# Kernel tuning notes

Hardware: AMD Instinct MI355X
Metric: run time of the kernel (lower is better)

Reference implementation:

```python
import jax, jax.numpy as jnp
import numpy as np

B, T, H, V, ADIM, AMAX = 16, 1024, 512, 32000, 512, 10


def setup_inputs() -> dict:
    key = jax.random.key(0)
    ks = jax.random.split(key, 24)
    def n(k, shape, s=0.05):
        return jax.random.normal(k, shape, jnp.float32) * s
    return {
        "instruction": jax.random.randint(ks[0], (B, T), 0, V, dtype=jnp.int32),
        "emb": n(ks[1], (V, H)),
        "wih_f": n(ks[2], (4 * H, H)), "whh_f": n(ks[3], (4 * H, H)),
        "bih_f": n(ks[4], (4 * H,)), "bhh_f": n(ks[5], (4 * H,)),
        "wih_b": n(ks[6], (4 * H, H)), "whh_b": n(ks[7], (4 * H, H)),
        "bih_b": n(ks[8], (4 * H,)), "bhh_b": n(ks[9], (4 * H,)),
        "wg": n(ks[10], (2 * H, 2 * H)), "bg": n(ks[11], (2 * H,)),
        "ws1": n(ks[12], (H, 2 * H)), "bs1": n(ks[13], (H,)),
        "ws2": n(ks[14], (1, H)), "bs2": n(ks[15], (1,)),
        "wd1": n(ks[16], (H, 2 * H)), "bd1": n(ks[17], (H,)),
        "wd2": n(ks[18], (ADIM, H)), "bd2": n(ks[19], (ADIM,)),
        "max_actions": AMAX,
    }


def _lstm(x, wih, whh, bias):
    # x: [B, T, H] -> outputs [B, T, H]; PyTorch gate order i, f, g, o
    h0 = jnp.zeros((x.shape[0], whh.shape[1]), x.dtype)
    def step(carry, xt):
        h, c = carry
        g = xt @ wih.T + h @ whh.T + bias
        i, f, gg, o = jnp.split(g, 4, axis=-1)
        c = jax.nn.sigmoid(f) * c + jax.nn.sigmoid(i) * jnp.tanh(gg)
        h = jax.nn.sigmoid(o) * jnp.tanh(c)
        return (h, c), h
    _, hs = jax.lax.scan(step, (h0, h0), jnp.swapaxes(x, 0, 1))
    return jnp.swapaxes(hs, 0, 1)


def reference(instruction, emb, wih_f, whh_f, bih_f, bhh_f, wih_b, whh_b, bih_b, bhh_b,
              wg, bg, ws1, bs1, ws2, bs2, wd1, bd1, wd2, bd2, max_actions):
    x = emb[instruction]                                   # [B, T, H]
    fwd = _lstm(x, wih_f, whh_f, bih_f + bhh_f)            # [B, T, H]
    bwd = _lstm(x[:, ::-1], wih_b, whh_b, bih_b + bhh_b)[:, ::-1]
    enc = jnp.concatenate([fwd, bwd], axis=-1)             # [B, T, 2H]
    # sequence_lengths=None: h_n[0]=fwd last step, h_n[1]=bwd at t=0
    pooled = jnp.concatenate([fwd[:, -1], bwd[:, 0]], axis=-1)
    gctx = pooled @ wg.T + bg                               # [B, 2H]
    sh = jax.nn.relu(enc @ ws1.T + bs1)
    seg_probs = jax.nn.sigmoid((sh @ ws2.T + bs2)[..., 0])  # [B, T]
    mask = seg_probs > 0.5
    count = mask.sum(axis=-1)
    # first max_actions True positions per row (stable sort keeps time order)
    order = jnp.argsort(jnp.logical_not(mask), axis=1, stable=True)[:, :max_actions]
    gathered = jnp.take_along_axis(enc, order[..., None], axis=1)  # [B, A, 2H]
    slots = jnp.arange(max_actions)
    valid = slots[None, :] < jnp.minimum(count, max_actions)[:, None]
    empty = ((count == 0)[:, None]) & (slots[None, :] == 0)  # fallback: decode global ctx
    dec_in = jnp.where(valid[..., None], gathered, 0.0)
    dec_in = jnp.where(empty[..., None], gctx[:, None, :], dec_in)
    dh = jax.nn.relu(dec_in @ wd1.T + bd1)
    actions = (dh @ wd2.T + bd2) * (valid | empty)[..., None].astype(dec_in.dtype)
    return actions, seg_probs
```

## Files before the change

### kernel.cpp

```cpp
#include <hip/hip_runtime.h>
#include <math.h>

#define T   1024
#define NB  16
#define HD  512

#define OFF_BAR  0
#define OFF_HH   256
#define OFF_SH   (OFF_HH + 16777216)
#define OFF_SEGP (OFF_SH + 8388608)
#define OFF_GCTX (OFF_SEGP + 16384)
#define OFF_SEL  (OFF_GCTX + 16384)

typedef unsigned long long u64;

__device__ __forceinline__ float sigmoidf_(float x){ return 1.0f/(1.0f + __expf(-x)); }
__device__ __forceinline__ float tanhf_(float x){ return 1.0f - 2.0f/(1.0f + __expf(2.0f*x)); }

__global__ __launch_bounds__(512, 1)
void lstm_kernel(const int* __restrict__ instr, const float* __restrict__ emb,
                 const float* __restrict__ wih_f, const float* __restrict__ whh_f,
                 const float* __restrict__ bih_f, const float* __restrict__ bhh_f,
                 const float* __restrict__ wih_b, const float* __restrict__ whh_b,
                 const float* __restrict__ bih_b, const float* __restrict__ bhh_b,
                 float* __restrict__ ws)
{
    float* h_hist = ws + OFF_HH;
    int* flags = (int*)ws;

    const int wg    = blockIdx.x;
    const int dir   = wg & 1;
    const int slice = wg >> 1;
    const int U     = slice * 4;

    int* barf = flags + dir*128;

    const float* wih = dir ? wih_b : wih_f;
    const float* whh = dir ? whh_b : whh_f;
    const float* bih = dir ? bih_b : bih_f;
    const float* bhh = dir ? bhh_b : bhh_f;

    const int tid  = threadIdx.x;
    const int wid  = tid >> 6;
    const int lane = tid & 63;
    const int bg   = wid >> 1;
    const int rg   = wid & 1;

    float wi[64], wh[64];
#pragma unroll
    for (int ri = 0; ri < 8; ++ri){
        int rgl = rg*8 + ri;
        int gate = rgl >> 2, unit = rgl & 3;
        size_t row = (size_t)(gate*HD + U + unit) * HD + lane*8;
        float4 a0 = *(const float4*)(wih + row);
        float4 a1 = *(const float4*)(wih + row + 4);
        float4 b0 = *(const float4*)(whh + row);
        float4 b1 = *(const float4*)(whh + row + 4);
        wi[ri*8+0]=a0.x; wi[ri*8+1]=a0.y; wi[ri*8+2]=a0.z; wi[ri*8+3]=a0.w;
        wi[ri*8+4]=a1.x; wi[ri*8+5]=a1.y; wi[ri*8+6]=a1.z; wi[ri*8+7]=a1.w;
        wh[ri*8+0]=b0.x; wh[ri*8+1]=b0.y; wh[ri*8+2]=b0.z; wh[ri*8+3]=b0.w;
        wh[ri*8+4]=b1.x; wh[ri*8+5]=b1.y; wh[ri*8+6]=b1.z; wh[ri*8+7]=b1.w;
    }

    float bI, bF, bG, bO, cst = 0.0f;
    {
        int u = tid & 3;
        bI = bih[0*HD + U + u] + bhh[0*HD + U + u];
        bF = bih[1*HD + U + u] + bhh[1*HD + U + u];
        bG = bih[2*HD + U + u] + bhh[2*HD + U + u];
        bO = bih[3*HD + U + u] + bhh[3*HD + U + u];
    }

    __shared__ float gbuf[256];

    const int jown = ((lane&1)<<4)|((lane&2)<<2)|(lane&4)|((lane&8)>>2)|((lane&16)>>4);
    const int own_bi  = jown >> 3;
    const int own_rgl = rg*8 + (jown & 7);
    const int gslot   = (own_rgl >> 2)*64 + (bg*4 + own_bi)*4 + (own_rgl & 3);

    for (int s = 0; s < T; ++s){
        const int tp = dir ? (T-1-s) : s;

        float a[32];
#pragma unroll
        for (int j = 0; j < 32; ++j) a[j] = 0.0f;

#pragma unroll
        for (int bi = 0; bi < 4; ++bi){
            int b = bg*4 + bi;
            int idx = instr[b*T + tp];
            const float* px = emb + (size_t)idx*HD + lane*8;
            float4 x0 = *(const float4*)px;
            float4 x1 = *(const float4*)(px + 4);
            float xs[8] = {x0.x,x0.y,x0.z,x0.w,x1.x,x1.y,x1.z,x1.w};
#pragma unroll
            for (int kk = 0; kk < 8; ++kk){
                float xv = xs[kk];
#pragma unroll
                for (int ri = 0; ri < 8; ++ri)
                    a[bi*8+ri] = fmaf(xv, wi[ri*8+kk], a[bi*8+ri]);
            }
        }

        if (s > 0){
            if (wid == 0){
                for (;;){
                    int v0 = __hip_atomic_load((int*)(barf + lane),      __ATOMIC_RELAXED, __HIP_MEMORY_SCOPE_AGENT);
                    int v1 = __hip_atomic_load((int*)(barf + 64 + lane), __ATOMIC_RELAXED, __HIP_MEMORY_SCOPE_AGENT);
                    if (__all((v0 >= s) && (v1 >= s))) break;
                    __builtin_amdgcn_s_sleep(1);
                }
            }
            __syncthreads();

            const int tprev = dir ? (T - s) : (s - 1);
            const float* hbase = h_hist + (size_t)(dir*T + tprev)*NB*HD;
#pragma unroll
            for (int bi = 0; bi < 4; ++bi){
                int b = bg*4 + bi;
                const float* ph = hbase + (size_t)b*HD + lane*8;
                float4 h0 = *(const float4*)ph;
                float4 h1 = *(const float4*)(ph + 4);
                float hs[8] = {h0.x,h0.y,h0.z,h0.w,h1.x,h1.y,h1.z,h1.w};
#pragma unroll
                for (int kk = 0; kk < 8; ++kk){
                    float hv = hs[kk];
#pragma unroll
                    for (int ri = 0; ri < 8; ++ri)
                        a[bi*8+ri] = fmaf(hv, wh[ri*8+kk], a[bi*8+ri]);
                }
            }
        }

#pragma unroll
        for (int m = 0; m < 5; ++m){
            const int half = 16 >> m;
            const bool up = (lane >> m) & 1;
#pragma unroll
            for (int j = 0; j < 16; ++j){
                if (j < half){
                    float lo = a[j], hi = a[j+half];
                    float rlo = __shfl_xor(lo, 1<<m, 64);
                    float rhi = __shfl_xor(hi, 1<<m, 64);
                    a[j] = up ? (hi + rhi) : (lo + rlo);
                }
            }
        }
        a[0] += __shfl_xor(a[0], 32, 64);

        if ((lane & 32) == 0) gbuf[gslot] = a[0];
        __syncthreads();

        if (tid < 64){
            float iv = sigmoidf_(gbuf[      tid] + bI);
            float fv = sigmoidf_(gbuf[ 64 + tid] + bF);
            float gv = tanhf_  (gbuf[128 + tid] + bG);
            float ov = sigmoidf_(gbuf[192 + tid] + bO);
            cst = fv*cst + iv*gv;
            float hv = ov * tanhf_(cst);
            int b = tid >> 2, u = tid & 3;
            __hip_atomic_store(&h_hist[((size_t)(dir*T + tp)*NB + b)*HD + U + u], hv,
                               __ATOMIC_RELAXED, __HIP_MEMORY_SCOPE_AGENT);
        }
        asm volatile("s_waitcnt vmcnt(0)" ::: "memory");
        __builtin_amdgcn_sched_barrier(0);
        if (tid == 0)
            __hip_atomic_store(barf + slice, s + 1, __ATOMIC_RELAXED, __HIP_MEMORY_SCOPE_AGENT);
    }
}

__global__ __launch_bounds__(256, 2)
void seg_gemm(const float* __restrict__ ws_, const float* __restrict__ ws1,
              const float* __restrict__ bs1)
{
    const float* h_hist = ws_ + OFF_HH;
    float* SH = (float*)(ws_ + OFF_SH);
    __shared__ float As[64][17];
    __shared__ float Bs[64][17];
    const int m0 = blockIdx.x * 64;
    const int n0 = blockIdx.y * 64;
    const int tid = threadIdx.x;
    const int r  = tid >> 2;
    const int kq = (tid & 3) * 4;
    const int ty = tid >> 4, tx = tid & 15;
    const int bI = m0 >> 10;
    const int t0 = m0 & 1023;

    float acc[4][4];
#pragma unroll
    for (int i=0;i<4;i++)
#pragma unroll
        for (int j=0;j<4;j++) acc[i][j]=0.0f;

    for (int kb = 0; kb < 1024; kb += 16){
        int kk = kb + kq;
        const float* ap = (kk < 512)
            ? h_hist + ((size_t)(t0 + r)*NB + bI)*HD + kk
            : h_hist + ((size_t)(T + t0 + r)*NB + bI)*HD + (kk - 512);
        float4 av = *(const float4*)ap;
        As[r][kq+0]=av.x; As[r][kq+1]=av.y; As[r][kq+2]=av.z; As[r][kq+3]=av.w;
        float4 bv = *(const float4*)(ws1 + (size_t)(n0 + r)*1024 + kk);
        Bs[r][kq+0]=bv.x; Bs[r][kq+1]=bv.y; Bs[r][kq+2]=bv.z; Bs[r][kq+3]=bv.w;
        __syncthreads();
#pragma unroll
        for (int k2 = 0; k2 < 16; ++k2){
            float av_[4], bv_[4];
#pragma unroll
            for (int i=0;i<4;i++) av_[i] = As[ty*4+i][k2];
#pragma unroll
            for (int j=0;j<4;j++) bv_[j] = Bs[tx*4+j][k2];
#pragma unroll
            for (int i=0;i<4;i++)
#pragma unroll
                for (int j=0;j<4;j++) acc[i][j] = fmaf(av_[i], bv_[j], acc[i][j]);
        }
        __syncthreads();
    }
#pragma unroll
    for (int i=0;i<4;i++){
        int m = m0 + ty*4 + i;
#pragma unroll
        for (int j=0;j<4;j++){
            int n = n0 + tx*4 + j;
            SH[(size_t)m*512 + n] = fmaxf(acc[i][j] + bs1[n], 0.0f);
        }
    }
}

__global__ void seg_score(const float* __restrict__ ws_, const float* __restrict__ ws2,
                          const float* __restrict__ bs2, float* __restrict__ dout)
{
    const float* SH = ws_ + OFF_SH;
    float* segp = (float*)(ws_ + OFF_SEGP);
    int row  = blockIdx.x*4 + (threadIdx.x >> 6);
    int lane = threadIdx.x & 63;
    const float* p = SH + (size_t)row*512 + lane*8;
    const float* q = ws2 + lane*8;
    float4 a0=*(const float4*)p, a1=*(const float4*)(p+4);
    float4 b0=*(const float4*)q, b1=*(const float4*)(q+4);
    float ssum = a0.x*b0.x + a0.y*b0.y + a0.z*b0.z + a0.w*b0.w
               + a1.x*b1.x + a1.y*b1.y + a1.z*b1.z + a1.w*b1.w;
#pragma unroll
    for (int m=1;m<64;m<<=1) ssum += __shfl_xor(ssum, m, 64);
    if (lane == 0){
        float z = ssum + bs2[0];
        float pr = 1.0f/(1.0f + __expf(-z));
        segp[row] = pr;
        dout[81920 + row] = pr;
    }
}

__global__ void select_gctx(float* __restrict__ ws_, const float* __restrict__ wgm,
                            const float* __restrict__ bgv)
{
    const float* h_hist = ws_ + OFF_HH;
    const float* segp   = ws_ + OFF_SEGP;
    float* gctx = ws_ + OFF_GCTX;
    int* sel = (int*)(ws_ + OFF_SEL);
    int b = blockIdx.x, tid = threadIdx.x;
    __shared__ unsigned char flag[1024];
    __shared__ float pool[1024];
    for (int j = tid; j < 1024; j += 256){
        flag[j] = segp[b*1024 + j] > 0.5f ? 1 : 0;
        pool[j] = (j < 512) ? h_hist[((size_t)1023*NB + b)*HD + j]
                            : h_hist[((size_t)T*NB + b)*HD + (j - 512)];
    }
    __syncthreads();
    if (tid == 0){
        int c = 0;
        int tmp[10];
        for (int j = 0; j < 10; ++j) tmp[j] = 0;
        for (int t = 0; t < 1024; ++t){
            if (flag[t]){ if (c < 10) tmp[c] = t; c++; }
        }
        for (int j = 0; j < 10; ++j) sel[b*12 + j] = tmp[j];
        sel[b*12 + 10] = c;
        sel[b*12 + 11] = 0;
    }
    __syncthreads();
    for (int n = tid; n < 1024; n += 256){
        float acc = bgv[n];
        const float* wr = wgm + (size_t)n*1024;
        for (int k = 0; k < 1024; k += 4){
            acc += wr[k]*pool[k] + wr[k+1]*pool[k+1] + wr[k+2]*pool[k+2] + wr[k+3]*pool[k+3];
        }
        gctx[b*1024 + n] = acc;
    }
}

__global__ void decode(const float* __restrict__ ws_, const float* __restrict__ wd1,
                       const float* __restrict__ bd1, const float* __restrict__ wd2,
                       const float* __restrict__ bd2, float* __restrict__ dout)
{
    const float* h_hist = ws_ + OFF_HH;
    const float* gctx   = ws_ + OFF_GCTX;
    const int* sel = (const int*)(ws_ + OFF_SEL);
    int blk = blockIdx.x;
    int b = blk / 10, slot = blk % 10;
    int tid = threadIdx.x;
    int count = sel[b*12 + 10];
    int nval = count < 10 ? count : 10;
    bool empty = (count == 0);
    float* outp = dout + (size_t)(b*10 + slot)*512;
    if (slot >= nval && !(empty && slot == 0)){
        for (int n = tid; n < 512; n += 256) outp[n] = 0.0f;
        return;
    }
    __shared__ float row[1024];
    __shared__ float dh[512];
    if (empty){
        for (int j = tid; j < 1024; j += 256) row[j] = gctx[b*1024 + j];
    } else {
        int t = sel[b*12 + slot];
        for (int j = tid; j < 1024; j += 256)
            row[j] = (j < 512) ? h_hist[((size_t)t*NB + b)*HD + j]
                               : h_hist[((size_t)(T + t)*NB + b)*HD + (j-512)];
    }
    __syncthreads();
    for (int d = tid; d < 512; d += 256){
        float acc = bd1[d];
        const float* wr = wd1 + (size_t)d*1024;
        for (int k = 0; k < 1024; ++k) acc += wr[k]*row[k];
        dh[d] = fmaxf(acc, 0.0f);
    }
    __syncthreads();
    for (int n = tid; n < 512; n += 256){
        float acc = bd2[n];
        const float* wr = wd2 + (size_t)n*512;
        for (int k = 0; k < 512; ++k) acc += wr[k]*dh[k];
        outp[n] = acc;
    }
}

extern "C" void kernel_launch(void* const* d_in, const int* in_sizes, int n_in,
                              void* d_out, int out_size, void* d_ws, size_t ws_size,
                              hipStream_t stream)
{
    const int*   instr = (const int*)d_in[0];
    const float* emb   = (const float*)d_in[1];
    const float* wih_f = (const float*)d_in[2];
    const float* whh_f = (const float*)d_in[3];
    const float* bih_f = (const float*)d_in[4];
    const float* bhh_f = (const float*)d_in[5];
    const float* wih_b = (const float*)d_in[6];
    const float* whh_b = (const float*)d_in[7];
    const float* bih_b = (const float*)d_in[8];
    const float* bhh_b = (const float*)d_in[9];
    const float* wg_   = (const float*)d_in[10];
    const float* bg_   = (const float*)d_in[11];
    const float* ws1   = (const float*)d_in[12];
    const float* bs1   = (const float*)d_in[13];
    const float* ws2   = (const float*)d_in[14];
    const float* bs2   = (const float*)d_in[15];
    const float* wd1   = (const float*)d_in[16];
    const float* bd1   = (const float*)d_in[17];
    const float* wd2   = (const float*)d_in[18];
    const float* bd2   = (const float*)d_in[19];
    float* out = (float*)d_out;
    float* ws  = (float*)d_ws;

    hipMemsetAsync(d_ws, 0, 1024, stream);

    hipLaunchKernelGGL(lstm_kernel, dim3(256), dim3(512), 0, stream,
                       instr, emb, wih_f, whh_f, bih_f, bhh_f,
                       wih_b, whh_b, bih_b, bhh_b, ws);
    hipLaunchKernelGGL(seg_gemm, dim3(256, 8), dim3(256), 0, stream, ws, ws1, bs1);
    hipLaunchKernelGGL(seg_score, dim3(4096), dim3(256), 0, stream, ws, ws2, bs2, out);
    hipLaunchKernelGGL(select_gctx, dim3(16), dim3(256), 0, stream, ws, wg_, bg_);
    hipLaunchKernelGGL(decode, dim3(160), dim3(256), 0, stream, ws, wd1, bd1, wd2, bd2, out);
}
```

Baseline: 4.749 ms.

## Remove block barriers from LSTM step via per-wave gate ownership and LDS counters

Reassigns weight rows so each wave holds all four gates for two units. The gate nonlinearity and cell update can then run inside each wave using lane shuffles, which removes the shared-memory gate buffer and the second __syncthreads per step. The global-flag wait now releases the other waves through an LDS spin variable instead of __syncthreads. An LDS atomic counter lets the last of the 8 waves publish the step flag. Input-projection FMAs are also interleaved with the h loads so they can hide memory latency. This risks memory-ordering subtleties, since the relaxed LDS spins and the counter reset carry no fences, and it adds spinning overhead.

```diff
diff --git a/kernel.cpp b/kernel.cpp
--- a/kernel.cpp
+++ b/kernel.cpp
@@ -44,14 +44,18 @@
     const int wid  = tid >> 6;
     const int lane = tid & 63;
     const int bg   = wid >> 1;
-    const int rg   = wid & 1;
+    const int ug   = wid & 1;
+
+    __shared__ int cnt[2];
+    __shared__ int release;
+    if (tid == 0){ cnt[0] = 0; cnt[1] = 0; release = 0; }
+    __syncthreads();
 
     float wi[64], wh[64];
 #pragma unroll
     for (int ri = 0; ri < 8; ++ri){
-        int rgl = rg*8 + ri;
-        int gate = rgl >> 2, unit = rgl & 3;
-        size_t row = (size_t)(gate*HD + U + unit) * HD + lane*8;
+        int gate = ri >> 1, ui = ri & 1;
+        size_t row = (size_t)(gate*HD + U + ug*2 + ui) * HD + lane*8;
         float4 a0 = *(const float4*)(wih + row);
         float4 a1 = *(const float4*)(wih + row + 4);
         float4 b0 = *(const float4*)(whh + row);
@@ -62,73 +66,121 @@
         wh[ri*8+4]=b1.x; wh[ri*8+5]=b1.y; wh[ri*8+6]=b1.z; wh[ri*8+7]=b1.w;
     }
 
-    float bI, bF, bG, bO, cst = 0.0f;
-    {
-        int u = tid & 3;
-        bI = bih[0*HD + U + u] + bhh[0*HD + U + u];
-        bF = bih[1*HD + U + u] + bhh[1*HD + U + u];
-        bG = bih[2*HD + U + u] + bhh[2*HD + U + u];
-        bO = bih[3*HD + U + u] + bhh[3*HD + U + u];
-    }
-
-    __shared__ float gbuf[256];
-
-    const int jown = ((lane&1)<<4)|((lane&2)<<2)|(lane&4)|((lane&8)>>2)|((lane&16)>>4);
-    const int own_bi  = jown >> 3;
-    const int own_rgl = rg*8 + (jown & 7);
-    const int gslot   = (own_rgl >> 2)*64 + (bg*4 + own_bi)*4 + (own_rgl & 3);
+    const int j5 = ((lane&1)<<4)|((lane&2)<<2)|(lane&4)|((lane&8)>>2)|((lane&16)>>4);
+    const int own_bi = j5 >> 3;
+    const int own_ui = j5 & 1;
+    const bool owner = (lane < 32) && ((lane & 12) == 0);
+    const int own_b  = bg*4 + own_bi;
+    const int own_u  = U + ug*2 + own_ui;
+
+    const float bI = bih[0*HD + own_u] + bhh[0*HD + own_u];
+    const float bF = bih[1*HD + own_u] + bhh[1*HD + own_u];
+    const float bG = bih[2*HD + own_u] + bhh[2*HD + own_u];
+    const float bO = bih[3*HD + own_u] + bhh[3*HD + own_u];
+    float cst = 0.0f;
 
     for (int s = 0; s < T; ++s){
         const int tp = dir ? (T-1-s) : s;
 
-        float a[32];
-#pragma unroll
-        for (int j = 0; j < 32; ++j) a[j] = 0.0f;
-
+        float4 xb[8];
 #pragma unroll
         for (int bi = 0; bi < 4; ++bi){
             int b = bg*4 + bi;
             int idx = instr[b*T + tp];
             const float* px = emb + (size_t)idx*HD + lane*8;
-            float4 x0 = *(const float4*)px;
-            float4 x1 = *(const float4*)(px + 4);
-            float xs[8] = {x0.x,x0.y,x0.z,x0.w,x1.x,x1.y,x1.z,x1.w};
-#pragma unroll
-            for (int kk = 0; kk < 8; ++kk){
-                float xv = xs[kk];
-#pragma unroll
-                for (int ri = 0; ri < 8; ++ri)
-                    a[bi*8+ri] = fmaf(xv, wi[ri*8+kk], a[bi*8+ri]);
-            }
+            xb[bi*2]   = *(const float4*)px;
+            xb[bi*2+1] = *(const float4*)(px + 4);
         }
 
         if (s > 0){
             if (wid == 0){
                 for (;;){
-                    int v0 = __hip_atomic_load((int*)(barf + lane),      __ATOMIC_RELAXED, __HIP_MEMORY_SCOPE_AGENT);
-                    int v1 = __hip_atomic_load((int*)(barf + 64 + lane), __ATOMIC_RELAXED, __HIP_MEMORY_SCOPE_AGENT);
+                    int v0 = __hip_atomic_load(barf + lane,      __ATOMIC_RELAXED, __HIP_MEMORY_SCOPE_AGENT);
+                    int v1 = __hip_atomic_load(barf + 64 + lane, __ATOMIC_RELAXED, __HIP_MEMORY_SCOPE_AGENT);
                     if (__all((v0 >= s) && (v1 >= s))) break;
                     __builtin_amdgcn_s_sleep(1);
                 }
-            }
-            __syncthreads();
-
-            const int tprev = dir ? (T - s) : (s - 1);
+                if (lane == 0)
+                    __hip_atomic_store(&release, s, __ATOMIC_RELAXED, __HIP_MEMORY_SCOPE_WORKGROUP);
+            }
+            while (__hip_atomic_load(&release, __ATOMIC_RELAXED, __HIP_MEMORY_SCOPE_WORKGROUP) < s) {}
+        }
+
+        float a[32];
+#pragma unroll
+        for (int j = 0; j < 32; ++j) a[j] = 0.0f;
+
+        if (s > 0){
+            const int tprev = dir ? (tp + 1) : (tp - 1);
             const float* hbase = h_hist + (size_t)(dir*T + tprev)*NB*HD;
+
+            const float* p0 = hbase + (size_t)(bg*4 + 0)*HD + lane*8;
+            const float* p1 = hbase + (size_t)(bg*4 + 1)*HD + lane*8;
+            float4 h00 = *(const float4*)p0, h01 = *(const float4*)(p0+4);
+            float4 h10 = *(const float4*)p1, h11 = *(const float4*)(p1+4);
+
+#pragma unroll
+            for (int bi = 0; bi < 2; ++bi){
+                float xs[8] = {xb[bi*2].x,xb[bi*2].y,xb[bi*2].z,xb[bi*2].w,
+                               xb[bi*2+1].x,xb[bi*2+1].y,xb[bi*2+1].z,xb[bi*2+1].w};
+#pragma unroll
+                for (int kk = 0; kk < 8; ++kk)
+#pragma unroll
+                    for (int ri = 0; ri < 8; ++ri)
+                        a[bi*8+ri] = fmaf(xs[kk], wi[ri*8+kk], a[bi*8+ri]);
+            }
+
+            const float* p2 = hbase + (size_t)(bg*4 + 2)*HD + lane*8;
+            const float* p3 = hbase + (size_t)(bg*4 + 3)*HD + lane*8;
+            float4 h20 = *(const float4*)p2, h21 = *(const float4*)(p2+4);
+            float4 h30 = *(const float4*)p3, h31 = *(const float4*)(p3+4);
+
+            {
+                float hs0[8] = {h00.x,h00.y,h00.z,h00.w,h01.x,h01.y,h01.z,h01.w};
+                float hs1[8] = {h10.x,h10.y,h10.z,h10.w,h11.x,h11.y,h11.z,h11.w};
+#pragma unroll
+                for (int kk = 0; kk < 8; ++kk){
+#pragma unroll
+                    for (int ri = 0; ri < 8; ++ri){
+                        a[0*8+ri] = fmaf(hs0[kk], wh[ri*8+kk], a[0*8+ri]);
+                        a[1*8+ri] = fmaf(hs1[kk], wh[ri*8+kk], a[1*8+ri]);
+                    }
+                }
+            }
+
+#pragma unroll
+            for (int bi = 2; bi < 4; ++bi){
+                float xs[8] = {xb[bi*2].x,xb[bi*2].y,xb[bi*2].z,xb[bi*2].w,
+                               xb[bi*2+1].x,xb[bi*2+1].y,xb[bi*2+1].z,xb[bi*2+1].w};
+#pragma unroll
+                for (int kk = 0; kk < 8; ++kk)
+#pragma unroll
+                    for (int ri = 0; ri < 8; ++ri)
+                        a[bi*8+ri] = fmaf(xs[kk], wi[ri*8+kk], a[bi*8+ri]);
+            }
+
+            {
+                float hs2[8] = {h20.x,h20.y,h20.z,h20.w,h21.x,h21.y,h21.z,h21.w};
+                float hs3[8] = {h30.x,h30.y,h30.z,h30.w,h31.x,h31.y,h31.z,h31.w};
+#pragma unroll
+                for (int kk = 0; kk < 8; ++kk){
+#pragma unroll
+                    for (int ri = 0; ri < 8; ++ri){
+                        a[2*8+ri] = fmaf(hs2[kk], wh[ri*8+kk], a[2*8+ri]);
+                        a[3*8+ri] = fmaf(hs3[kk], wh[ri*8+kk], a[3*8+ri]);
+                    }
+                }
+            }
+        } else {
 #pragma unroll
             for (int bi = 0; bi < 4; ++bi){
-                int b = bg*4 + bi;
-                const float* ph = hbase + (size_t)b*HD + lane*8;
-                float4 h0 = *(const float4*)ph;
-                float4 h1 = *(const float4*)(ph + 4);
-                float hs[8] = {h0.x,h0.y,h0.z,h0.w,h1.x,h1.y,h1.z,h1.w};
-#pragma unroll
-                for (int kk = 0; kk < 8; ++kk){
-                    float hv = hs[kk];
+                float xs[8] = {xb[bi*2].x,xb[bi*2].y,xb[bi*2].z,xb[bi*2].w,
+                               xb[bi*2+1].x,xb[bi*2+1].y,xb[bi*2+1].z,xb[bi*2+1].w};
+#pragma unroll
+                for (int kk = 0; kk < 8; ++kk)
 #pragma unroll
                     for (int ri = 0; ri < 8; ++ri)
-                        a[bi*8+ri] = fmaf(hv, wh[ri*8+kk], a[bi*8+ri]);
-                }
+                        a[bi*8+ri] = fmaf(xs[kk], wi[ri*8+kk], a[bi*8+ri]);
             }
         }
 
@@ -137,35 +189,42 @@
             const int half = 16 >> m;
             const bool up = (lane >> m) & 1;
 #pragma unroll
-            for (int j = 0; j < 16; ++j){
-                if (j < half){
-                    float lo = a[j], hi = a[j+half];
+            for (int jj = 0; jj < 16; ++jj){
+                if (jj < half){
+                    float lo = a[jj], hi = a[jj+half];
                     float rlo = __shfl_xor(lo, 1<<m, 64);
                     float rhi = __shfl_xor(hi, 1<<m, 64);
-                    a[j] = up ? (hi + rhi) : (lo + rlo);
+                    a[jj] = up ? (hi + rhi) : (lo + rlo);
                 }
             }
         }
         a[0] += __shfl_xor(a[0], 32, 64);
 
-        if ((lane & 32) == 0) gbuf[gslot] = a[0];
-        __syncthreads();
-
-        if (tid < 64){
-            float iv = sigmoidf_(gbuf[      tid] + bI);
-            float fv = sigmoidf_(gbuf[ 64 + tid] + bF);
-            float gv = tanhf_  (gbuf[128 + tid] + bG);
-            float ov = sigmoidf_(gbuf[192 + tid] + bO);
-            cst = fv*cst + iv*gv;
-            float hv = ov * tanhf_(cst);
-            int b = tid >> 2, u = tid & 3;
-            __hip_atomic_store(&h_hist[((size_t)(dir*T + tp)*NB + b)*HD + U + u], hv,
+        float vi = a[0];
+        float vf = __shfl_xor(vi, 8, 64);
+        float vg = __shfl_xor(vi, 4, 64);
+        float vo = __shfl_xor(vi, 12, 64);
+
+        float iv = sigmoidf_(vi + bI);
+        float fv = sigmoidf_(vf + bF);
+        float gv = tanhf_  (vg + bG);
+        float ov = sigmoidf_(vo + bO);
+        cst = fv*cst + iv*gv;
+        float hv = ov * tanhf_(cst);
+
+        if (owner)
+            __hip_atomic_store(&h_hist[((size_t)(dir*T + tp)*NB + own_b)*HD + own_u], hv,
                                __ATOMIC_RELAXED, __HIP_MEMORY_SCOPE_AGENT);
-        }
+
         asm volatile("s_waitcnt vmcnt(0)" ::: "memory");
         __builtin_amdgcn_sched_barrier(0);
-        if (tid == 0)
-            __hip_atomic_store(barf + slice, s + 1, __ATOMIC_RELAXED, __HIP_MEMORY_SCOPE_AGENT);
+        if (lane == 0){
+            int prev = atomicAdd(&cnt[s & 1], 1);
+            if (prev == 7){
+                cnt[s & 1] = 0;
+                __hip_atomic_store(barf + slice, s + 1, __ATOMIC_RELAXED, __HIP_MEMORY_SCOPE_AGENT);
+            }
+        }
     }
 }
 
```

Measured after the change: 9.343 ms. 96.8% more time.

## Prefetch next-step embedding rows into double-buffered LDS with async loads

Applied to the files above, without the earlier changes.

The recurrent LSTM kernel now gathers each step's embedding rows into a double-buffered shared-memory tile using global_load_lds, issued right after the step's flag store so they land during the next barrier wait. The input-projection FMAs move after the barrier and read from LDS. The previous-h loads are hoisted so all eight float4 loads are in flight before any FMAs run. This aims to take global embedding-gather latency off the serial per-step critical path, but it puts the input-projection FMAs back on that path and uses 64KB of LDS.

```diff
diff --git a/kernel.cpp b/kernel.cpp
--- a/kernel.cpp
+++ b/kernel.cpp
@@ -13,6 +13,8 @@
 #define OFF_SEL  (OFF_GCTX + 16384)
 
 typedef unsigned long long u64;
+typedef __attribute__((address_space(1))) const unsigned int gu32_t;
+typedef __attribute__((address_space(3))) unsigned int lu32_t;
 
 __device__ __forceinline__ float sigmoidf_(float x){ return 1.0f/(1.0f + __expf(-x)); }
 __device__ __forceinline__ float tanhf_(float x){ return 1.0f - 2.0f/(1.0f + __expf(2.0f*x)); }
@@ -45,6 +47,30 @@
     const int lane = tid & 63;
     const int bg   = wid >> 1;
     const int rg   = wid & 1;
+
+    __shared__ float x_lds[2][8192];
+    __shared__ float gbuf[256];
+
+#define ISSUE_FILLS(BUF, TN)                                                        \
+    if (wid > 0){                                                                   \
+        float* dstb = &x_lds[BUF][0];                                               \
+        _Pragma("unroll")                                                           \
+        for (int j = 0; j < 5; ++j){                                                \
+            int q = j*7 + wid - 1;                                                  \
+            if (q < 32){                                                            \
+                int b_ = q >> 1;                                                    \
+                int idxv = instr[b_*T + (TN)];                                      \
+                const float* src = emb + (size_t)idxv*HD + (2*lane + (q&1))*4;      \
+                __builtin_amdgcn_global_load_lds((gu32_t*)(const void*)src,         \
+                    (lu32_t*)(void*)(dstb + q*256), 16, 0, 0);                      \
+            }                                                                       \
+        }                                                                           \
+    }
+
+    {
+        int t0 = dir ? (T-1) : 0;
+        ISSUE_FILLS(0, t0)
+    }
 
     float wi[64], wh[64];
 #pragma unroll
@@ -71,63 +97,103 @@
         bO = bih[3*HD + U + u] + bhh[3*HD + U + u];
     }
 
-    __shared__ float gbuf[256];
-
     const int jown = ((lane&1)<<4)|((lane&2)<<2)|(lane&4)|((lane&8)>>2)|((lane&16)>>4);
     const int own_bi  = jown >> 3;
     const int own_rgl = rg*8 + (jown & 7);
     const int gslot   = (own_rgl >> 2)*64 + (bg*4 + own_bi)*4 + (own_rgl & 3);
 
+    asm volatile("s_waitcnt vmcnt(0)" ::: "memory");
+    __builtin_amdgcn_sched_barrier(0);
+    __syncthreads();
+
     for (int s = 0; s < T; ++s){
         const int tp = dir ? (T-1-s) : s;
-
-        float a[32];
-#pragma unroll
-        for (int j = 0; j < 32; ++j) a[j] = 0.0f;
-
-#pragma unroll
-        for (int bi = 0; bi < 4; ++bi){
-            int b = bg*4 + bi;
-            int idx = instr[b*T + tp];
-            const float* px = emb + (size_t)idx*HD + lane*8;
-            float4 x0 = *(const float4*)px;
-            float4 x1 = *(const float4*)(px + 4);
-            float xs[8] = {x0.x,x0.y,x0.z,x0.w,x1.x,x1.y,x1.z,x1.w};
-#pragma unroll
-            for (int kk = 0; kk < 8; ++kk){
-                float xv = xs[kk];
-#pragma unroll
-                for (int ri = 0; ri < 8; ++ri)
-                    a[bi*8+ri] = fmaf(xv, wi[ri*8+kk], a[bi*8+ri]);
-            }
-        }
+        const int cur = s & 1;
 
         if (s > 0){
             if (wid == 0){
                 for (;;){
-                    int v0 = __hip_atomic_load((int*)(barf + lane),      __ATOMIC_RELAXED, __HIP_MEMORY_SCOPE_AGENT);
-                    int v1 = __hip_atomic_load((int*)(barf + 64 + lane), __ATOMIC_RELAXED, __HIP_MEMORY_SCOPE_AGENT);
+                    int v0 = __hip_atomic_load(barf + lane,      __ATOMIC_RELAXED, __HIP_MEMORY_SCOPE_AGENT);
+                    int v1 = __hip_atomic_load(barf + 64 + lane, __ATOMIC_RELAXED, __HIP_MEMORY_SCOPE_AGENT);
                     if (__all((v0 >= s) && (v1 >= s))) break;
                     __builtin_amdgcn_s_sleep(1);
                 }
             }
+            asm volatile("s_waitcnt vmcnt(0)" ::: "memory");
+            __builtin_amdgcn_sched_barrier(0);
             __syncthreads();
-
+        }
+
+        float a[32];
+#pragma unroll
+        for (int j = 0; j < 32; ++j) a[j] = 0.0f;
+
+        if (s > 0){
             const int tprev = dir ? (T - s) : (s - 1);
             const float* hbase = h_hist + (size_t)(dir*T + tprev)*NB*HD;
+            const float* p0 = hbase + (size_t)(bg*4 + 0)*HD + lane*8;
+            const float* p1 = hbase + (size_t)(bg*4 + 1)*HD + lane*8;
+            const float* p2 = hbase + (size_t)(bg*4 + 2)*HD + lane*8;
+            const float* p3 = hbase + (size_t)(bg*4 + 3)*HD + lane*8;
+            float4 h00 = *(const float4*)p0, h01 = *(const float4*)(p0+4);
+            float4 h10 = *(const float4*)p1, h11 = *(const float4*)(p1+4);
+            float4 h20 = *(const float4*)p2, h21 = *(const float4*)(p2+4);
+            float4 h30 = *(const float4*)p3, h31 = *(const float4*)(p3+4);
+
+            const float* xl = &x_lds[cur][0];
 #pragma unroll
             for (int bi = 0; bi < 4; ++bi){
                 int b = bg*4 + bi;
-                const float* ph = hbase + (size_t)b*HD + lane*8;
-                float4 h0 = *(const float4*)ph;
-                float4 h1 = *(const float4*)(ph + 4);
-                float hs[8] = {h0.x,h0.y,h0.z,h0.w,h1.x,h1.y,h1.z,h1.w};
+                float4 x0 = *(const float4*)&xl[b*512 + lane*4];
+                float4 x1 = *(const float4*)&xl[b*512 + 256 + lane*4];
+                float xs[8] = {x0.x,x0.y,x0.z,x0.w,x1.x,x1.y,x1.z,x1.w};
 #pragma unroll
                 for (int kk = 0; kk < 8; ++kk){
-                    float hv = hs[kk];
+                    float xv = xs[kk];
 #pragma unroll
                     for (int ri = 0; ri < 8; ++ri)
-                        a[bi*8+ri] = fmaf(hv, wh[ri*8+kk], a[bi*8+ri]);
+                        a[bi*8+ri] = fmaf(xv, wi[ri*8+kk], a[bi*8+ri]);
+                }
+            }
+
+            {
+                float hs0[8] = {h00.x,h00.y,h00.z,h00.w,h01.x,h01.y,h01.z,h01.w};
+                float hs1[8] = {h10.x,h10.y,h10.z,h10.w,h11.x,h11.y,h11.z,h11.w};
+#pragma unroll
+                for (int kk = 0; kk < 8; ++kk){
+#pragma unroll
+                    for (int ri = 0; ri < 8; ++ri){
+                        a[0*8+ri] = fmaf(hs0[kk], wh[ri*8+kk], a[0*8+ri]);
+                        a[1*8+ri] = fmaf(hs1[kk], wh[ri*8+kk], a[1*8+ri]);
+                    }
+                }
+            }
+            {
+                float hs2[8] = {h20.x,h20.y,h20.z,h20.w,h21.x,h21.y,h21.z,h21.w};
+                float hs3[8] = {h30.x,h30.y,h30.z,h30.w,h31.x,h31.y,h31.z,h31.w};
+#pragma unroll
+                for (int kk = 0; kk < 8; ++kk){
+#pragma unroll
+                    for (int ri = 0; ri < 8; ++ri){
+                        a[2*8+ri] = fmaf(hs2[kk], wh[ri*8+kk], a[2*8+ri]);
+                        a[3*8+ri] = fmaf(hs3[kk], wh[ri*8+kk], a[3*8+ri]);
+                    }
+                }
+            }
+        } else {
+            const float* xl = &x_lds[cur][0];
+#pragma unroll
+            for (int bi = 0; bi < 4; ++bi){
+                int b = bg*4 + bi;
+                float4 x0 = *(const float4*)&xl[b*512 + lane*4];
+                float4 x1 = *(const float4*)&xl[b*512 + 256 + lane*4];
+                float xs[8] = {x0.x,x0.y,x0.z,x0.w,x1.x,x1.y,x1.z,x1.w};
+#pragma unroll
+                for (int kk = 0; kk < 8; ++kk){
+                    float xv = xs[kk];
+#pragma unroll
+                    for (int ri = 0; ri < 8; ++ri)
+                        a[bi*8+ri] = fmaf(xv, wi[ri*8+kk], a[bi*8+ri]);
                 }
             }
         }
@@ -166,6 +232,11 @@
         __builtin_amdgcn_sched_barrier(0);
         if (tid == 0)
             __hip_atomic_store(barf + slice, s + 1, __ATOMIC_RELAXED, __HIP_MEMORY_SCOPE_AGENT);
+
+        if (s + 1 < T){
+            int tn = dir ? (T-2-s) : (s+1);
+            ISSUE_FILLS(cur ^ 1, tn)
+        }
     }
 }
 
```

Result: slower. 7.364 ms (+55.1%).

## Split LSTM workgroups by batch group to shrink barrier fan-in

Applied to the files above, without the earlier changes.

Workgroups are re-partitioned so each one handles 16 hidden units for 4 batch rows, instead of 4 units for all 16 rows. Each direction now uses 4 independent barrier groups of 32 workgroups rather than one group of 128. Each workgroup therefore waits on only 32 flags per step instead of 128, which cuts the spin-wait cost and the coupling across the recurrence. The trade-off is that each workgroup loads 4× more distinct weight rows per batch group, and the total workgroup count and register use are unchanged.

```diff
diff --git a/kernel.cpp b/kernel.cpp
--- a/kernel.cpp
+++ b/kernel.cpp
@@ -28,12 +28,14 @@
     float* h_hist = ws + OFF_HH;
     int* flags = (int*)ws;
 
-    const int wg    = blockIdx.x;
-    const int dir   = wg & 1;
-    const int slice = wg >> 1;
-    const int U     = slice * 4;
-
-    int* barf = flags + dir*128;
+    const int wg     = blockIdx.x;
+    const int dir    = wg & 1;
+    const int bgrp   = (wg >> 1) & 3;
+    const int uslice = wg >> 3;
+    const int U      = uslice * 16;
+    const int b0     = bgrp * 4;
+
+    int* barf = flags + (dir*4 + bgrp)*32;
 
     const float* wih = dir ? wih_b : wih_f;
     const float* whh = dir ? whh_b : whh_f;
@@ -43,28 +45,27 @@
     const int tid  = threadIdx.x;
     const int wid  = tid >> 6;
     const int lane = tid & 63;
-    const int bg   = wid >> 1;
-    const int rg   = wid & 1;
+    const int rg   = wid;
 
     float wi[64], wh[64];
 #pragma unroll
     for (int ri = 0; ri < 8; ++ri){
         int rgl = rg*8 + ri;
-        int gate = rgl >> 2, unit = rgl & 3;
-        size_t row = (size_t)(gate*HD + U + unit) * HD + lane*8;
+        int gate = rgl >> 4, ul = rgl & 15;
+        size_t row = (size_t)(gate*HD + U + ul) * HD + lane*8;
         float4 a0 = *(const float4*)(wih + row);
         float4 a1 = *(const float4*)(wih + row + 4);
-        float4 b0 = *(const float4*)(whh + row);
-        float4 b1 = *(const float4*)(whh + row + 4);
+        float4 b0v = *(const float4*)(whh + row);
+        float4 b1v = *(const float4*)(whh + row + 4);
         wi[ri*8+0]=a0.x; wi[ri*8+1]=a0.y; wi[ri*8+2]=a0.z; wi[ri*8+3]=a0.w;
         wi[ri*8+4]=a1.x; wi[ri*8+5]=a1.y; wi[ri*8+6]=a1.z; wi[ri*8+7]=a1.w;
-        wh[ri*8+0]=b0.x; wh[ri*8+1]=b0.y; wh[ri*8+2]=b0.z; wh[ri*8+3]=b0.w;
-        wh[ri*8+4]=b1.x; wh[ri*8+5]=b1.y; wh[ri*8+6]=b1.z; wh[ri*8+7]=b1.w;
+        wh[ri*8+0]=b0v.x; wh[ri*8+1]=b0v.y; wh[ri*8+2]=b0v.z; wh[ri*8+3]=b0v.w;
+        wh[ri*8+4]=b1v.x; wh[ri*8+5]=b1v.y; wh[ri*8+6]=b1v.z; wh[ri*8+7]=b1v.w;
     }
 
     float bI, bF, bG, bO, cst = 0.0f;
     {
-        int u = tid & 3;
+        int u = tid & 15;
         bI = bih[0*HD + U + u] + bhh[0*HD + U + u];
         bF = bih[1*HD + U + u] + bhh[1*HD + U + u];
         bG = bih[2*HD + U + u] + bhh[2*HD + U + u];
@@ -76,7 +77,7 @@
     const int jown = ((lane&1)<<4)|((lane&2)<<2)|(lane&4)|((lane&8)>>2)|((lane&16)>>4);
     const int own_bi  = jown >> 3;
     const int own_rgl = rg*8 + (jown & 7);
-    const int gslot   = (own_rgl >> 2)*64 + (bg*4 + own_bi)*4 + (own_rgl & 3);
+    const int gslot   = (own_rgl >> 4)*64 + own_bi*16 + (own_rgl & 15);
 
     for (int s = 0; s < T; ++s){
         const int tp = dir ? (T-1-s) : s;
@@ -87,7 +88,7 @@
 
 #pragma unroll
         for (int bi = 0; bi < 4; ++bi){
-            int b = bg*4 + bi;
+            int b = b0 + bi;
             int idx = instr[b*T + tp];
             const float* px = emb + (size_t)idx*HD + lane*8;
             float4 x0 = *(const float4*)px;
@@ -105,9 +106,8 @@
         if (s > 0){
             if (wid == 0){
                 for (;;){
-                    int v0 = __hip_atomic_load((int*)(barf + lane),      __ATOMIC_RELAXED, __HIP_MEMORY_SCOPE_AGENT);
-                    int v1 = __hip_atomic_load((int*)(barf + 64 + lane), __ATOMIC_RELAXED, __HIP_MEMORY_SCOPE_AGENT);
-                    if (__all((v0 >= s) && (v1 >= s))) break;
+                    int v = __hip_atomic_load(barf + (lane & 31), __ATOMIC_RELAXED, __HIP_MEMORY_SCOPE_AGENT);
+                    if (__all(v >= s)) break;
                     __builtin_amdgcn_s_sleep(1);
                 }
             }
@@ -117,7 +117,7 @@
             const float* hbase = h_hist + (size_t)(dir*T + tprev)*NB*HD;
 #pragma unroll
             for (int bi = 0; bi < 4; ++bi){
-                int b = bg*4 + bi;
+                int b = b0 + bi;
                 const float* ph = hbase + (size_t)b*HD + lane*8;
                 float4 h0 = *(const float4*)ph;
                 float4 h1 = *(const float4*)(ph + 4);
@@ -158,14 +158,14 @@
             float ov = sigmoidf_(gbuf[192 + tid] + bO);
             cst = fv*cst + iv*gv;
             float hv = ov * tanhf_(cst);
-            int b = tid >> 2, u = tid & 3;
+            int b = b0 + (tid >> 4), u = tid & 15;
             __hip_atomic_store(&h_hist[((size_t)(dir*T + tp)*NB + b)*HD + U + u], hv,
                                __ATOMIC_RELAXED, __HIP_MEMORY_SCOPE_AGENT);
         }
         asm volatile("s_waitcnt vmcnt(0)" ::: "memory");
         __builtin_amdgcn_sched_barrier(0);
         if (tid == 0)
-            __hip_atomic_store(barf + slice, s + 1, __ATOMIC_RELAXED, __HIP_MEMORY_SCOPE_AGENT);
+            __hip_atomic_store(barf + uslice, s + 1, __ATOMIC_RELAXED, __HIP_MEMORY_SCOPE_AGENT);
     }
 }
 
```

Measured after the change: 4.465 ms. -6.0%, faster.
